# Kernel tuning notes

Measured on AMD Instinct MI355X. Metric: run time of the kernel, lower is better.

## Reference

```python
import jax, jax.numpy as jnp
import numpy as np

DIM = 2048
HEADS = 16
DIM_HEAD = 128
DIM_INNER = HEADS * DIM_HEAD  # 2048
EPS = 1.1920929e-07  # torch RMSNorm default eps = finfo(float32).eps


def setup_inputs() -> dict:
    key = jax.random.key(0)
    k_tok, k_q, k_kv, k_o = jax.random.split(key, 4)
    tokens = jax.random.normal(k_tok, (4, 2048, DIM), dtype=jnp.float32)
    # Linear weights stored as [in, out]; torch init ~ U(-1/sqrt(in), 1/sqrt(in)), use scaled normal
    s = 0.02
    w_q = jax.random.normal(k_q, (DIM, DIM_INNER), dtype=jnp.float32) * s
    w_kv = jax.random.normal(k_kv, (DIM, 2 * DIM_INNER), dtype=jnp.float32) * s
    w_out = jax.random.normal(k_o, (DIM_INNER, DIM), dtype=jnp.float32) * s
    norm_weight = jnp.ones((DIM,), dtype=jnp.float32)
    return {"tokens": tokens, "norm_weight": norm_weight, "w_q": w_q, "w_kv": w_kv, "w_out": w_out}


def _rmsnorm(x, weight):
    var = jnp.mean(jnp.square(x), axis=-1, keepdims=True)
    return x * jax.lax.rsqrt(var + EPS) * weight


def reference(tokens, norm_weight, w_q, w_kv, w_out):
    b, n, _ = tokens.shape
    x = _rmsnorm(tokens, norm_weight)
    q = x @ w_q                       # [b, n, h*d]
    kv = x @ w_kv                     # [b, n, 2*h*d]
    k, v = jnp.split(kv, 2, axis=-1)

    def split_heads(t):
        return t.reshape(b, n, HEADS, DIM_HEAD).transpose(0, 2, 1, 3)  # b h n d

    q, k, v = map(split_heads, (q, k, v))
    q = q * (DIM_HEAD ** -0.5)
    sim = jnp.einsum('bhid,bhjd->bhij', q, k)
    attn = jax.nn.softmax(sim, axis=-1)
    out = jnp.einsum('bhij,bhjd->bhid', attn, v)
    out = out.transpose(0, 2, 1, 3).reshape(b, n, DIM_INNER)
    return out @ w_out
```

## Files before the change

### kernel.cpp

```cpp
#include <hip/hip_runtime.h>
#include <hip/hip_bf16.h>
#include <stdint.h>

#define SEQ   2048
#define DIM   2048
#define HEADS 16
#define DHEAD 128
#define BATCH 4
#define MROWS (BATCH*SEQ)

typedef short bf16x8 __attribute__((ext_vector_type(8)));
typedef float f32x4  __attribute__((ext_vector_type(4)));
typedef float f32x16 __attribute__((ext_vector_type(16)));
typedef unsigned short u16x8 __attribute__((ext_vector_type(8)));
typedef unsigned int u32x4 __attribute__((ext_vector_type(4)));

__device__ __forceinline__ short f2bf(float f){
  union { float fv; unsigned u; } x; x.fv = f;
  unsigned r = x.u + 0x7fffu + ((x.u >> 16) & 1u);
  return (short)(r >> 16);
}

__device__ __forceinline__ unsigned cvtpk(float lo, float hi){
  unsigned r; asm("v_cvt_pk_bf16_f32 %0, %1, %2" : "=v"(r) : "v"(lo), "v"(hi)); return r;
}

__device__ __forceinline__ float exp2a(float x){
#if __has_builtin(__builtin_amdgcn_exp2f)
  return __builtin_amdgcn_exp2f(x);
#else
  return exp2f(x);
#endif
}

__device__ __forceinline__ void gl_lds16(const void* g, void* l){
  __builtin_amdgcn_global_load_lds((const __attribute__((address_space(1))) void*)g,
                                   (__attribute__((address_space(3))) void*)l, 16, 0, 0);
}

__global__ __launch_bounds__(256) void rmsnorm_cast_k(const float* __restrict__ tok,
                                                      const float* __restrict__ w,
                                                      short* __restrict__ x){
  const int row = blockIdx.x;
  const float4* r4 = (const float4*)(tok + (size_t)row * DIM);
  float4 a = r4[threadIdx.x * 2];
  float4 b = r4[threadIdx.x * 2 + 1];
  float ss = a.x*a.x + a.y*a.y + a.z*a.z + a.w*a.w
           + b.x*b.x + b.y*b.y + b.z*b.z + b.w*b.w;
  #pragma unroll
  for (int m = 1; m < 64; m <<= 1) ss += __shfl_xor(ss, m, 64);
  __shared__ float red[4];
  if ((threadIdx.x & 63) == 0) red[threadIdx.x >> 6] = ss;
  __syncthreads();
  float tot = red[0] + red[1] + red[2] + red[3];
  float rs = rsqrtf(tot * (1.0f / DIM) + 1.1920929e-07f);
  const float4* w4 = (const float4*)w;
  float4 wa = w4[threadIdx.x * 2];
  float4 wb = w4[threadIdx.x * 2 + 1];
  u16x8 o;
  o[0] = (unsigned short)f2bf(a.x * rs * wa.x);
  o[1] = (unsigned short)f2bf(a.y * rs * wa.y);
  o[2] = (unsigned short)f2bf(a.z * rs * wa.z);
  o[3] = (unsigned short)f2bf(a.w * rs * wa.w);
  o[4] = (unsigned short)f2bf(b.x * rs * wb.x);
  o[5] = (unsigned short)f2bf(b.y * rs * wb.y);
  o[6] = (unsigned short)f2bf(b.z * rs * wb.z);
  o[7] = (unsigned short)f2bf(b.w * rs * wb.w);
  *(u16x8*)(x + (size_t)row * DIM + threadIdx.x * 8) = o;
}

__global__ __launch_bounds__(256) void wtrans_k(const float* __restrict__ w,
                                                short* __restrict__ wt,
                                                int K, int N){
  __shared__ float tile[64][65];
  const int r0 = blockIdx.y * 64;
  const int c0 = blockIdx.x * 64;
  const int t = threadIdx.x;
  #pragma unroll
  for (int i = 0; i < 16; i++){
    int e = i * 256 + t; int r = e >> 6, c = e & 63;
    tile[r][c] = w[(size_t)(r0 + r) * N + c0 + c];
  }
  __syncthreads();
  #pragma unroll
  for (int i = 0; i < 16; i++){
    int e = i * 256 + t; int c = e >> 6, r = e & 63;
    wt[(size_t)(c0 + c) * K + r0 + r] = f2bf(tile[r][c]);
  }
}

__global__ __launch_bounds__(256) void vtrans_k(const short* __restrict__ kv,
                                                short* __restrict__ vt){
  __shared__ short tile[64][65];
  const int n0 = blockIdx.x * 64;
  const int d0 = blockIdx.y * 64;
  const int bh = blockIdx.z;
  const int b = bh >> 4, h = bh & 15;
  const int t = threadIdx.x;
  #pragma unroll
  for (int i = 0; i < 16; i++){
    int e = i * 256 + t; int r = e >> 6, c = e & 63;
    tile[r][c] = kv[(size_t)(b * SEQ + n0 + r) * 4096 + 2048 + h * DHEAD + d0 + c];
  }
  __syncthreads();
  #pragma unroll
  for (int i = 0; i < 16; i++){
    int e = i * 256 + t; int c = e >> 6, r = e & 63;
    vt[(size_t)(bh * DHEAD + d0 + c) * SEQ + n0 + r] = tile[r][c];
  }
}

__device__ __forceinline__ void storeC(float* C, size_t idx, float v){ C[idx] = v; }
__device__ __forceinline__ void storeC(short* C, size_t idx, float v){ C[idx] = f2bf(v); }

template<typename OutT>
__global__ __launch_bounds__(512, 2) void gemm256_k(const short* __restrict__ A,
                                                    const short* __restrict__ Bt,
                                                    OutT* __restrict__ C,
                                                    int M, int N, int K, int lgntn){
  __shared__ __align__(16) short As[4][256 * 32];
  __shared__ __align__(16) short Bs[4][256 * 32];
  const int nwg = gridDim.x;
  const int bid = blockIdx.x;
  const int o = (bid & 7) * (nwg >> 3) + (bid >> 3);
  const int bm = o >> lgntn, bn = o & ((1 << lgntn) - 1);
  const int m0 = bm << 8, n0 = bn << 8;
  const int tid = threadIdx.x, lane = tid & 63, wid = tid >> 6;
  const int l31 = lane & 31, hi = lane >> 5;
  const int wr = wid >> 2, wc = wid & 3;
  const int NT = K >> 5;

  f32x16 acc[4][2] = {};

  auto stage = [&](int t){
    const int slot = t & 3;
    const size_t kbase = (size_t)t << 5;
    #pragma unroll
    for (int i = 0; i < 2; i++){
      int c = i * 512 + tid;
      int row = c >> 2;
      int j = (c & 3) ^ ((row >> 1) & 3);
      gl_lds16(A + (size_t)(m0 + row) * K + kbase + j * 8,
               &As[slot][(i * 512 + wid * 64) * 8]);
    }
    #pragma unroll
    for (int i = 0; i < 2; i++){
      int c = i * 512 + tid;
      int row = c >> 2;
      int j = (c & 3) ^ ((row >> 1) & 3);
      gl_lds16(Bt + (size_t)(n0 + row) * K + kbase + j * 8,
               &Bs[slot][(i * 512 + wid * 64) * 8]);
    }
  };

  auto compute = [&](int t){
    const short* Ab = As[t & 3];
    const short* Bb = Bs[t & 3];
    bf16x8 af[4][2], bfv[2][2];
    #pragma unroll
    for (int mb = 0; mb < 4; mb++){
      int row = wr * 128 + mb * 32 + l31;
      #pragma unroll
      for (int ks = 0; ks < 2; ks++){
        int ch = (ks * 2 + hi) ^ ((row >> 1) & 3);
        af[mb][ks] = *(const bf16x8*)&Ab[row * 32 + ch * 8];
      }
    }
    #pragma unroll
    for (int nb = 0; nb < 2; nb++){
      int row = wc * 64 + nb * 32 + l31;
      #pragma unroll
      for (int ks = 0; ks < 2; ks++){
        int ch = (ks * 2 + hi) ^ ((row >> 1) & 3);
        bfv[nb][ks] = *(const bf16x8*)&Bb[row * 32 + ch * 8];
      }
    }
    __builtin_amdgcn_s_setprio(1);
    #pragma unroll
    for (int mb = 0; mb < 4; mb++)
      #pragma unroll
      for (int nb = 0; nb < 2; nb++)
        #pragma unroll
        for (int ks = 0; ks < 2; ks++)
          acc[mb][nb] = __builtin_amdgcn_mfma_f32_32x32x16_bf16(af[mb][ks], bfv[nb][ks],
                                                                acc[mb][nb], 0, 0, 0);
    __builtin_amdgcn_s_setprio(0);
  };

  stage(0); stage(1); stage(2);
  asm volatile("s_waitcnt vmcnt(8)" ::: "memory");
  __builtin_amdgcn_s_barrier();

  for (int t = 0; t < NT; t++){
    if (t + 3 < NT) stage(t + 3);
    compute(t);
    if (t + 1 < NT){
      if (t + 3 < NT)      asm volatile("s_waitcnt vmcnt(8)" ::: "memory");
      else if (t + 2 < NT) asm volatile("s_waitcnt vmcnt(4)" ::: "memory");
      else                 asm volatile("s_waitcnt vmcnt(0)" ::: "memory");
      __builtin_amdgcn_s_barrier();
    }
  }

  #pragma unroll
  for (int mb = 0; mb < 4; mb++)
    #pragma unroll
    for (int nb = 0; nb < 2; nb++)
      #pragma unroll
      for (int reg = 0; reg < 16; reg++){
        int r = (reg & 3) + 8 * (reg >> 2) + 4 * hi;
        int row = m0 + wr * 128 + mb * 32 + r;
        int col = n0 + wc * 64 + nb * 32 + l31;
        storeC(C, (size_t)row * N + col, acc[mb][nb][reg]);
      }
}

__global__ __launch_bounds__(256) void attn_k(const short* __restrict__ q,
                                              const short* __restrict__ kv,
                                              const short* __restrict__ vt,
                                              short* __restrict__ out){
  __shared__ __align__(16) short Ks[2][64 * 128];
  __shared__ __align__(16) short Vts[2][128 * 64];
  const int qt = blockIdx.x, bh = blockIdx.y;
  const int b = bh >> 4, h = bh & 15;
  const int tid = threadIdx.x, lane = tid & 63, wid = tid >> 6;
  const int l31 = lane & 31, hi = lane >> 5;
  const int qrow0 = qt * 128 + wid * 32;
  const float c2 = 0.08838834764831845f * 1.4426950408889634f;
  const int NT = SEQ / 64;

  bf16x8 qf[8];
  {
    const short* qp = q + (size_t)(b * SEQ + qrow0 + l31) * DIM + h * DHEAD + hi * 8;
    #pragma unroll
    for (int s = 0; s < 8; s++) qf[s] = *(const bf16x8*)(qp + s * 16);
  }

  f32x16 acc[4] = {};
  float m2 = -3e38f, l_s = 0.f;

  auto stage = [&](int kt, int bs){
    #pragma unroll
    for (int i = 0; i < 4; i++){
      int cb = (i * 4 + wid) * 64;
      int c  = cb + lane;
      int kr = c >> 4, kj = (c & 15) ^ (kr & 7);
      gl_lds16(kv + (size_t)(b * SEQ + kt * 64 + kr) * 4096 + h * DHEAD + kj * 8,
               &Ks[bs][cb * 8]);
      int vr = c >> 3, vj = (c & 7) ^ (vr & 7);
      gl_lds16(vt + (size_t)(bh * DHEAD + vr) * SEQ + kt * 64 + vj * 8,
               &Vts[bs][cb * 8]);
    }
  };

  stage(0, 0);
  int cur = 0;

  for (int kt = 0; kt < NT; kt++){
    if (kt + 1 < NT){
      stage(kt + 1, cur ^ 1);
      asm volatile("s_waitcnt vmcnt(8)" ::: "memory");
    } else {
      asm volatile("s_waitcnt vmcnt(0)" ::: "memory");
    }
    __builtin_amdgcn_s_barrier();

    const short* Kb = Ks[cur];
    const short* Vb = Vts[cur];

    f32x16 t0 = {0,0,0,0,0,0,0,0,0,0,0,0,0,0,0,0};
    f32x16 t1 = t0;
    {
      const int r0 = l31, r1 = l31 + 32;
      #pragma unroll
      for (int s = 0; s < 8; s++){
        bf16x8 k0 = *(const bf16x8*)&Kb[r0 * 128 + (((2 * s + hi) ^ (r0 & 7)) * 8)];
        bf16x8 k1 = *(const bf16x8*)&Kb[r1 * 128 + (((2 * s + hi) ^ (r1 & 7)) * 8)];
        t0 = __builtin_amdgcn_mfma_f32_32x32x16_bf16(k0, qf[s], t0, 0, 0, 0);
        t1 = __builtin_amdgcn_mfma_f32_32x32x16_bf16(k1, qf[s], t1, 0, 0, 0);
      }
    }

    float mxr = t0[0];
    #pragma unroll
    for (int i = 1; i < 16; i++) mxr = fmaxf(mxr, t0[i]);
    #pragma unroll
    for (int i = 0; i < 16; i++) mxr = fmaxf(mxr, t1[i]);
    mxr = fmaxf(mxr, __shfl_xor(mxr, 32));
    float mx2 = mxr * c2;
    if (!__all(mx2 <= m2 + 11.5f)){
      float m2n = fmaxf(m2, mx2);
      float al = exp2a(m2 - m2n);
      m2 = m2n;
      l_s *= al;
      #pragma unroll
      for (int reg = 0; reg < 16; reg++){
        float ar = __shfl(al, (reg & 3) + 8 * (reg >> 2) + 4 * hi);
        #pragma unroll
        for (int dt = 0; dt < 4; dt++) acc[dt][reg] *= ar;
      }
    }

    float ps = 0.f;
    unsigned w[16];
    #pragma unroll
    for (int pr = 0; pr < 8; pr++){
      float pa_ = exp2a(fmaf(t0[2 * pr], c2, -m2));
      float pb_ = exp2a(fmaf(t0[2 * pr + 1], c2, -m2));
      ps += pa_ + pb_;
      w[pr] = cvtpk(pa_, pb_);
    }
    #pragma unroll
    for (int pr = 0; pr < 8; pr++){
      float pa_ = exp2a(fmaf(t1[2 * pr], c2, -m2));
      float pb_ = exp2a(fmaf(t1[2 * pr + 1], c2, -m2));
      ps += pa_ + pb_;
      w[8 + pr] = cvtpk(pa_, pb_);
    }
    ps += __shfl_xor(ps, 32);
    l_s += ps;

    #pragma unroll
    for (int fp = 0; fp < 4; fp++){
      unsigned A0 = w[fp * 4 + 0], A1 = w[fp * 4 + 1];
      unsigned B0 = w[fp * 4 + 2], B1 = w[fp * 4 + 3];
      unsigned xA0 = __shfl_xor((int)A0, 32), xA1 = __shfl_xor((int)A1, 32);
      unsigned xB0 = __shfl_xor((int)B0, 32), xB1 = __shfl_xor((int)B1, 32);
      u32x4 fw;
      fw[0] = hi ? xB0 : A0;
      fw[1] = hi ? xB1 : A1;
      fw[2] = hi ? B0 : xA0;
      fw[3] = hi ? B1 : xA1;
      union { u32x4 u; bf16x8 v; } pc; pc.u = fw;
      #pragma unroll
      for (int dt = 0; dt < 4; dt++){
        int vr = dt * 32 + l31;
        bf16x8 vb = *(const bf16x8*)&Vb[vr * 64 + (((2 * fp + hi) ^ (vr & 7)) * 8)];
        acc[dt] = __builtin_amdgcn_mfma_f32_32x32x16_bf16(pc.v, vb, acc[dt], 0, 0, 0);
      }
    }

    asm volatile("s_waitcnt lgkmcnt(0)" ::: "memory");
    __builtin_amdgcn_s_barrier();
    cur ^= 1;
  }

  float inv = 1.0f / l_s;
  #pragma unroll
  for (int reg = 0; reg < 16; reg++){
    int cr = (reg & 3) + 8 * (reg >> 2) + 4 * hi;
    float li = __shfl(inv, cr);
    int row = qrow0 + cr;
    #pragma unroll
    for (int dt = 0; dt < 4; dt++)
      out[(size_t)(b * SEQ + row) * DIM + h * DHEAD + dt * 32 + l31] = f2bf(acc[dt][reg] * li);
  }
}

extern "C" void kernel_launch(void* const* d_in, const int* in_sizes, int n_in,
                              void* d_out, int out_size, void* d_ws, size_t ws_size,
                              hipStream_t stream) {
  (void)in_sizes; (void)n_in; (void)out_size; (void)ws_size;
  const float* tokens = (const float*)d_in[0];
  const float* normw  = (const float*)d_in[1];
  const float* wq     = (const float*)d_in[2];
  const float* wkv    = (const float*)d_in[3];
  const float* wout   = (const float*)d_in[4];
  float* outp = (float*)d_out;
  char* ws = (char*)d_ws;

  short* x     = (short*)(ws + 0);
  short* wqt   = (short*)(ws + 33554432);
  short* wkvt  = (short*)(ws + 41943040);
  short* woutt = (short*)(ws + 58720256);
  short* qb    = (short*)(ws + 67108864);
  short* kvb   = (short*)(ws + 100663296);
  short* vtb   = (short*)(ws + 167772160);

  rmsnorm_cast_k<<<dim3(MROWS), dim3(256), 0, stream>>>(tokens, normw, x);
  wtrans_k<<<dim3(2048/64, 2048/64), dim3(256), 0, stream>>>(wq,   wqt,   2048, 2048);
  wtrans_k<<<dim3(4096/64, 2048/64), dim3(256), 0, stream>>>(wkv,  wkvt,  2048, 4096);
  wtrans_k<<<dim3(2048/64, 2048/64), dim3(256), 0, stream>>>(wout, woutt, 2048, 2048);
  gemm256_k<short><<<dim3((MROWS/256)*(2048/256)), dim3(512), 0, stream>>>(x, wqt,  qb,  MROWS, 2048, 2048, 3);
  gemm256_k<short><<<dim3((MROWS/256)*(4096/256)), dim3(512), 0, stream>>>(x, wkvt, kvb, MROWS, 4096, 2048, 4);
  vtrans_k<<<dim3(SEQ/64, DHEAD/64, BATCH*HEADS), dim3(256), 0, stream>>>(kvb, vtb);
  attn_k<<<dim3(SEQ/128, BATCH*HEADS), dim3(256), 0, stream>>>(qb, kvb, vtb, qb);
  gemm256_k<float><<<dim3((MROWS/256)*(2048/256)), dim3(512), 0, stream>>>(qb, woutt, outp, MROWS, 2048, 2048, 3);
}
```

Before: 610.9 us.

## Interleave GEMM global-to-LDS staging with per-row-block MFMA phases; widen K swizzle

The GEMM main loop now splits each tile's global-to-LDS staging into four quarter loads, issuing one per row-block phase so the loads interleave with MFMA work. Each phase also gets an extra barrier and scheduling fences. Separately, the attention kernel's K-tile LDS swizzle widens from 3 to 4 bits to cut bank conflicts, and a sched fence is placed after the Q load. The extra per-phase barriers add synchronisation cost that may offset the overlap gained.

```diff
diff --git a/kernel.cpp b/kernel.cpp
--- a/kernel.cpp
+++ b/kernel.cpp
@@ -36,6 +36,11 @@
 __device__ __forceinline__ void gl_lds16(const void* g, void* l){
   __builtin_amdgcn_global_load_lds((const __attribute__((address_space(1))) void*)g,
                                    (__attribute__((address_space(3))) void*)l, 16, 0, 0);
+}
+
+__device__ __forceinline__ void ofence(){
+  asm volatile("" ::: "memory");
+  __builtin_amdgcn_sched_barrier(0);
 }
 
 __global__ __launch_bounds__(256) void rmsnorm_cast_k(const float* __restrict__ tok,
@@ -132,68 +137,72 @@
 
   f32x16 acc[4][2] = {};
 
-  auto stage = [&](int t){
+  auto stageQ = [&](int t, int q){
     const int slot = t & 3;
     const size_t kbase = (size_t)t << 5;
-    #pragma unroll
-    for (int i = 0; i < 2; i++){
-      int c = i * 512 + tid;
+    if (q < 2){
+      int c = q * 512 + tid;
       int row = c >> 2;
       int j = (c & 3) ^ ((row >> 1) & 3);
       gl_lds16(A + (size_t)(m0 + row) * K + kbase + j * 8,
-               &As[slot][(i * 512 + wid * 64) * 8]);
-    }
-    #pragma unroll
-    for (int i = 0; i < 2; i++){
-      int c = i * 512 + tid;
+               &As[slot][(q * 512 + wid * 64) * 8]);
+    } else {
+      int c = (q - 2) * 512 + tid;
       int row = c >> 2;
       int j = (c & 3) ^ ((row >> 1) & 3);
       gl_lds16(Bt + (size_t)(n0 + row) * K + kbase + j * 8,
-               &Bs[slot][(i * 512 + wid * 64) * 8]);
+               &Bs[slot][((q - 2) * 512 + wid * 64) * 8]);
     }
   };
 
-  auto compute = [&](int t){
+  #pragma unroll
+  for (int t = 0; t < 3; t++){
+    #pragma unroll
+    for (int q = 0; q < 4; q++) stageQ(t, q);
+    ofence();
+  }
+  asm volatile("s_waitcnt vmcnt(8)" ::: "memory");
+  __builtin_amdgcn_s_barrier();
+
+  for (int t = 0; t < NT; t++){
     const short* Ab = As[t & 3];
     const short* Bb = Bs[t & 3];
-    bf16x8 af[4][2], bfv[2][2];
-    #pragma unroll
-    for (int mb = 0; mb < 4; mb++){
-      int row = wr * 128 + mb * 32 + l31;
-      #pragma unroll
-      for (int ks = 0; ks < 2; ks++){
-        int ch = (ks * 2 + hi) ^ ((row >> 1) & 3);
-        af[mb][ks] = *(const bf16x8*)&Ab[row * 32 + ch * 8];
-      }
-    }
-    #pragma unroll
-    for (int nb = 0; nb < 2; nb++){
-      int row = wc * 64 + nb * 32 + l31;
-      #pragma unroll
-      for (int ks = 0; ks < 2; ks++){
-        int ch = (ks * 2 + hi) ^ ((row >> 1) & 3);
-        bfv[nb][ks] = *(const bf16x8*)&Bb[row * 32 + ch * 8];
-      }
-    }
-    __builtin_amdgcn_s_setprio(1);
-    #pragma unroll
-    for (int mb = 0; mb < 4; mb++)
+    bf16x8 bfv[2][2];
+
+    #pragma unroll
+    for (int p = 0; p < 4; p++){
+      if (p == 0){
+        #pragma unroll
+        for (int nb = 0; nb < 2; nb++){
+          int row = wc * 64 + nb * 32 + l31;
+          #pragma unroll
+          for (int ks = 0; ks < 2; ks++){
+            int ch = (ks * 2 + hi) ^ ((row >> 1) & 3);
+            bfv[nb][ks] = *(const bf16x8*)&Bb[row * 32 + ch * 8];
+          }
+        }
+      }
+      bf16x8 af[2];
+      {
+        int row = wr * 128 + p * 32 + l31;
+        #pragma unroll
+        for (int ks = 0; ks < 2; ks++){
+          int ch = (ks * 2 + hi) ^ ((row >> 1) & 3);
+          af[ks] = *(const bf16x8*)&Ab[row * 32 + ch * 8];
+        }
+      }
+      if (t + 3 < NT){ stageQ(t + 3, p); ofence(); }
+      __builtin_amdgcn_s_barrier();
+      __builtin_amdgcn_s_setprio(1);
       #pragma unroll
       for (int nb = 0; nb < 2; nb++)
         #pragma unroll
         for (int ks = 0; ks < 2; ks++)
-          acc[mb][nb] = __builtin_amdgcn_mfma_f32_32x32x16_bf16(af[mb][ks], bfv[nb][ks],
-                                                                acc[mb][nb], 0, 0, 0);
-    __builtin_amdgcn_s_setprio(0);
-  };
-
-  stage(0); stage(1); stage(2);
-  asm volatile("s_waitcnt vmcnt(8)" ::: "memory");
-  __builtin_amdgcn_s_barrier();
-
-  for (int t = 0; t < NT; t++){
-    if (t + 3 < NT) stage(t + 3);
-    compute(t);
+          acc[p][nb] = __builtin_amdgcn_mfma_f32_32x32x16_bf16(af[ks], bfv[nb][ks],
+                                                               acc[p][nb], 0, 0, 0);
+      __builtin_amdgcn_s_setprio(0);
+    }
+
     if (t + 1 < NT){
       if (t + 3 < NT)      asm volatile("s_waitcnt vmcnt(8)" ::: "memory");
       else if (t + 2 < NT) asm volatile("s_waitcnt vmcnt(4)" ::: "memory");
@@ -235,6 +244,7 @@
     #pragma unroll
     for (int s = 0; s < 8; s++) qf[s] = *(const bf16x8*)(qp + s * 16);
   }
+  ofence();
 
   f32x16 acc[4] = {};
   float m2 = -3e38f, l_s = 0.f;
@@ -244,7 +254,7 @@
     for (int i = 0; i < 4; i++){
       int cb = (i * 4 + wid) * 64;
       int c  = cb + lane;
-      int kr = c >> 4, kj = (c & 15) ^ (kr & 7);
+      int kr = c >> 4, kj = (c & 15) ^ (kr & 15);
       gl_lds16(kv + (size_t)(b * SEQ + kt * 64 + kr) * 4096 + h * DHEAD + kj * 8,
                &Ks[bs][cb * 8]);
       int vr = c >> 3, vj = (c & 7) ^ (vr & 7);
@@ -274,8 +284,8 @@
       const int r0 = l31, r1 = l31 + 32;
       #pragma unroll
       for (int s = 0; s < 8; s++){
-        bf16x8 k0 = *(const bf16x8*)&Kb[r0 * 128 + (((2 * s + hi) ^ (r0 & 7)) * 8)];
-        bf16x8 k1 = *(const bf16x8*)&Kb[r1 * 128 + (((2 * s + hi) ^ (r1 & 7)) * 8)];
+        bf16x8 k0 = *(const bf16x8*)&Kb[r0 * 128 + (((2 * s + hi) ^ (r0 & 15)) * 8)];
+        bf16x8 k1 = *(const bf16x8*)&Kb[r1 * 128 + (((2 * s + hi) ^ (r1 & 15)) * 8)];
         t0 = __builtin_amdgcn_mfma_f32_32x32x16_bf16(k0, qf[s], t0, 0, 0, 0);
         t1 = __builtin_amdgcn_mfma_f32_32x32x16_bf16(k1, qf[s], t1, 0, 0, 0);
       }
```

New measurement: 613.9 us. About the same (+0.5%).
